# Optimization experiments

Hardware: AMD Instinct MI355X
Metric: run time of the kernel (lower is better)

The kernel has to match this reference:

```python
import jax, jax.numpy as jnp
import numpy as np

BLK = 64          # BLOCK_M == BLOCK_N == 64
TOPK_RATIO = 0.25


def _block_map(q, k, topk):
    # mean_pool of q blocks and mean-centered k blocks, then top-k key blocks per query block
    B, H, L, D = q.shape
    nb = L // BLK
    k_cent = k - jnp.mean(k, axis=-2, keepdims=True)
    pq = q.reshape(B, H, nb, BLK, D).mean(axis=3)          # [B,H,Mb,D]
    pk = k_cent.reshape(B, H, nb, BLK, D).mean(axis=3)     # [B,H,Nb,D]
    score = jnp.einsum('bhmd,bhnd->bhmn', pq, pk)
    _, lut = jax.lax.top_k(score, topk)                    # [B,H,Mb,topk] int32
    return lut


def reference(q, k, v):
    B, H, L, D = q.shape
    nb = L // BLK                       # M_BLOCKS == N_BLOCKS (L divisible by 64)
    topk = min(nb, int(TOPK_RATIO * nb))
    qk_scale = D ** (-0.5)

    lut = jax.lax.stop_gradient(_block_map(q, k, topk))    # routing is non-differentiable

    qb = q.reshape(B, H, nb, BLK, D)
    kb = k.reshape(B, H, nb, BLK, D)
    vb = v.reshape(B, H, nb, BLK, D)

    # gather selected key/value blocks per query block: [B,H,Mb,topk,BLK,D]
    idx = lut[:, :, :, :, None, None]
    k_sel = jnp.take_along_axis(kb[:, :, None], idx, axis=3)
    v_sel = jnp.take_along_axis(vb[:, :, None], idx, axis=3)

    # block-sparse attention restricted to the selected blocks
    s = jnp.einsum('bhmqd,bhmtkd->bhmqtk', qb, k_sel) * qk_scale
    s = s.reshape(B, H, nb, BLK, topk * BLK)
    p = jax.nn.softmax(s, axis=-1)                         # online-softmax equivalent
    v_flat = v_sel.reshape(B, H, nb, topk * BLK, D)
    o = jnp.einsum('bhmqn,bhmnd->bhmqd', p, v_flat)
    return o.reshape(B, H, L, D)


def setup_inputs() -> dict:
    key = jax.random.key(0)
    k1, k2, k3 = jax.random.split(key, 3)
    shape = (2, 8, 4096, 64)
    return {
        'q': jax.random.normal(k1, shape, dtype=jnp.float32),
        'k': jax.random.normal(k2, shape, dtype=jnp.float32),
        'v': jax.random.normal(k3, shape, dtype=jnp.float32),
    }
```

## Files before the change

kernel.cpp:

```cpp
#include <hip/hip_runtime.h>
#include <hip/hip_bf16.h>

#define B_ 2
#define H_ 8
#define L_ 4096
#define D_ 64
#define NB_ 64
#define TOPK_ 16
#define BH_ 16

typedef __bf16 bf16x8 __attribute__((ext_vector_type(8)));
typedef float f32x4 __attribute__((ext_vector_type(4)));

#if __has_builtin(__builtin_amdgcn_exp2f)
#define EXP2(x) __builtin_amdgcn_exp2f(x)
#else
#define EXP2(x) exp2f(x)
#endif

__global__ __launch_bounds__(256) void prep_all_kernel(
    const float* __restrict__ q, const float* __restrict__ k,
    const float* __restrict__ v,
    float* __restrict__ pq, float* __restrict__ pk,
    __bf16* __restrict__ kimg, __bf16* __restrict__ vimg) {
  const int tid = threadIdx.x;
  if (blockIdx.x < BH_ * NB_) {
    const int blk = blockIdx.x;
    const int bh = blk >> 6, m = blk & 63;
    const int d = tid & 63, g = tid >> 6;
    const float* qb = q + ((size_t)bh * L_ + m * 64 + g * 16) * D_ + d;
    float sq = 0.f;
#pragma unroll
    for (int i = 0; i < 16; i++) sq += qb[(size_t)i * D_];
    __shared__ float bufq[4][64];
    bufq[g][d] = sq;
    __syncthreads();
    if (g == 0) {
      float tq = bufq[0][d] + bufq[1][d] + bufq[2][d] + bufq[3][d];
      pq[(size_t)blk * 64 + d] = tq * (1.f / 64.f);
    }
  } else if (blockIdx.x < 2 * BH_ * NB_) {
    const int blk = blockIdx.x - BH_ * NB_;
    const int srow = tid >> 2;
    const int sc16 = (tid & 3) * 16;
    __shared__ __align__(16) float s_kf[64][64];
    __shared__ __align__(16) __bf16 s_kt[4096];

    const float* ks = k + (size_t)blk * 4096 + srow * 64 + sc16;
    float kf[16];
#pragma unroll
    for (int h = 0; h < 4; h++) {
      float4 t4 = *(const float4*)(ks + h * 4);
      kf[h * 4 + 0] = t4.x; kf[h * 4 + 1] = t4.y; kf[h * 4 + 2] = t4.z; kf[h * 4 + 3] = t4.w;
      *(float4*)&s_kf[srow][sc16 + h * 4] = t4;
    }

#pragma unroll
    for (int h = 0; h < 2; h++) {
      const int d0 = sc16 + h * 8;
      const int i = (d0 >> 5) * 4 + (srow >> 4);
      const int ln = ((d0 >> 3) & 3) * 16 + (srow & 15);
      bf16x8 kw;
#pragma unroll
      for (int j = 0; j < 8; j++) kw[j] = (__bf16)kf[h * 8 + j];
      *(bf16x8*)&s_kt[(i * 64 + ln) * 8] = kw;
    }
    __syncthreads();

    __bf16* gk = kimg + (size_t)blk * 4096;
    *(bf16x8*)(gk + tid * 8)        = *(const bf16x8*)(s_kt + tid * 8);
    *(bf16x8*)(gk + 2048 + tid * 8) = *(const bf16x8*)(s_kt + 2048 + tid * 8);

    const int d = tid & 63, g = tid >> 6;
    float sk = 0.f;
#pragma unroll
    for (int i = 0; i < 16; i++) sk += s_kf[g * 16 + i][d];
    __shared__ float bufk[4][64];
    bufk[g][d] = sk;
    __syncthreads();
    if (g == 0) {
      float tk = bufk[0][d] + bufk[1][d] + bufk[2][d] + bufk[3][d];
      pk[(size_t)blk * 64 + d] = tk * (1.f / 64.f);
    }
  } else {
    const int blk = blockIdx.x - 2 * BH_ * NB_;
    const int srow = tid >> 2;
    const int sc16 = (tid & 3) * 16;

    const float* vs = v + (size_t)blk * 4096 + srow * 64 + sc16;
    float vf[16];
#pragma unroll
    for (int h = 0; h < 4; h++) {
      float4 u4 = *(const float4*)(vs + h * 4);
      vf[h * 4 + 0] = u4.x; vf[h * 4 + 1] = u4.y; vf[h * 4 + 2] = u4.z; vf[h * 4 + 3] = u4.w;
    }

    const int kpos = (srow & 32) + ((srow >> 2) & 3) * 8 + ((srow >> 4) & 1) * 4 + (srow & 3);
    __shared__ __align__(16) __bf16 s_vt[4096];
#pragma unroll
    for (int i = 0; i < 16; i++) {
      int d = sc16 + i;
      s_vt[d * 64 + kpos] = (__bf16)vf[i];
    }
    __syncthreads();
    __bf16* gv = vimg + (size_t)blk * 4096;
#pragma unroll
    for (int h = 0; h < 2; h++) {
      int c = tid + h * 256;
      int i = c >> 6, ln = c & 63;
      int ct2 = i & 3, s2 = i >> 2;
      int d = ct2 * 16 + (ln & 15), c8 = s2 * 4 + (ln >> 4);
      *(bf16x8*)(gv + c * 8) = *(const bf16x8*)(s_vt + d * 64 + c8 * 8);
    }
  }
}

__global__ __launch_bounds__(256) void blockmap_kernel(
    const float* __restrict__ pq, const float* __restrict__ pk,
    int* __restrict__ lut) {
  const int g = blockIdx.x;
  const int bh = g >> 2, q4 = g & 3;
  const int t = threadIdx.x;
  const int lane = t & 63, w = t >> 6;

  __shared__ float s_pk[64][65];
  __shared__ float s_km[64];
  __shared__ float s_pq[16][64];
  __shared__ float s_sc[4][64];

#pragma unroll
  for (int i = 0; i < 16; i++) {
    int idx = i * 256 + t;
    s_pk[idx >> 6][idx & 63] = pk[(size_t)bh * 4096 + idx];
  }
#pragma unroll
  for (int i = 0; i < 4; i++) {
    int idx = i * 256 + t;
    s_pq[idx >> 6][idx & 63] = pq[(size_t)bh * 4096 + q4 * 1024 + idx];
  }
  __syncthreads();
  if (t < 64) {
    float s = 0.f;
#pragma unroll 8
    for (int r = 0; r < 64; r++) s += s_pk[r][t];
    s_km[t] = s * (1.f / 64.f);
  }
  __syncthreads();

#pragma unroll
  for (int rr = 0; rr < 4; rr++) {
    const int row = w * 4 + rr;
    float sc = 0.f;
#pragma unroll 8
    for (int d2 = 0; d2 < 64; ++d2)
      sc += s_pq[row][d2] * (s_pk[lane][d2] - s_km[d2]);
    s_sc[w][lane] = sc;
    __syncthreads();
    int rank = 0;
#pragma unroll 8
    for (int j = 0; j < 64; j++) {
      float o = s_sc[w][j];
      rank += (o > sc) || (o == sc && j < lane);
    }
    if (rank < TOPK_)
      lut[((size_t)bh * 64 + q4 * 16 + row) * TOPK_ + rank] = lane;
    __syncthreads();
  }
}

__global__ __launch_bounds__(256, 4) void sparse_attn_fast(
    const float* __restrict__ q, const __bf16* __restrict__ kimg,
    const __bf16* __restrict__ vimg, const float* __restrict__ pq,
    const float* __restrict__ pk, float* __restrict__ out) {
  const int bid = blockIdx.x;
  const int blk = (bid & 7) * 128 + (bid >> 3);
  const int bh = blk >> 6, m = blk & 63;
  const int tid = threadIdx.x;
  const int lane = tid & 63;
  const int w = tid >> 6;
  const int l16 = lane & 15, lhi = lane >> 4;

  __shared__ float s_pk[64][65];
  __shared__ float s_km[64];
  __shared__ float s_pqr[64];
  __shared__ float s_sc[64];
  __shared__ int s_lut[TOPK_];

  {
    const float* pkb = pk + (size_t)bh * 4096;
#pragma unroll
    for (int i = 0; i < 16; i++) {
      int idx = i * 256 + tid;
      s_pk[idx >> 6][idx & 63] = pkb[idx];
    }
    if (tid < 64) s_pqr[tid] = pq[((size_t)bh * 64 + m) * 64 + tid];
    __syncthreads();
    if (tid < 64) {
      float s = 0.f;
#pragma unroll 8
      for (int r = 0; r < 64; r++) s += s_pk[r][tid];
      s_km[tid] = s * (1.f / 64.f);
    }
    __syncthreads();
    float sc = 0.f;
#pragma unroll 8
    for (int d2 = 0; d2 < 64; ++d2)
      sc += s_pqr[d2] * (s_pk[lane][d2] - s_km[d2]);
    s_sc[lane] = sc;
    __syncthreads();
    int rank = 0;
#pragma unroll 8
    for (int j = 0; j < 64; j++) {
      float o = s_sc[j];
      rank += (o > sc) || (o == sc && j < lane);
    }
    if (rank < TOPK_) s_lut[rank] = lane;
    __syncthreads();
  }

  const size_t base = (size_t)bh * L_ * D_;
  const __bf16* kbase = kimg + (size_t)bh * 64 * 4096;
  const __bf16* vbase = vimg + (size_t)bh * 64 * 4096;

  const float QSC = 0.125f * 1.44269504088896340736f;
  bf16x8 qf[2];
  {
    const float* qrow = q + base + (size_t)(m * 64 + w * 16 + l16) * D_;
#pragma unroll
    for (int s = 0; s < 2; s++) {
      const float* p0 = qrow + s * 32 + lhi * 8;
      float4 a = *(const float4*)p0;
      float4 b = *(const float4*)(p0 + 4);
      bf16x8 f;
      f[0] = (__bf16)(a.x * QSC); f[1] = (__bf16)(a.y * QSC);
      f[2] = (__bf16)(a.z * QSC); f[3] = (__bf16)(a.w * QSC);
      f[4] = (__bf16)(b.x * QSC); f[5] = (__bf16)(b.y * QSC);
      f[6] = (__bf16)(b.z * QSC); f[7] = (__bf16)(b.w * QSC);
      qf[s] = f;
    }
  }

  f32x4 acc_o[4];
#pragma unroll
  for (int i = 0; i < 4; i++) acc_o[i] = (f32x4){0.f, 0.f, 0.f, 0.f};
  float l_run = 0.f;

  for (int it = 0; it < TOPK_; ++it) {
    const int kb = s_lut[it];

    const __bf16* gk = kbase + (size_t)kb * 4096 + lane * 8;
    const __bf16* gv = vbase + (size_t)kb * 4096 + lane * 8;
    bf16x8 kf[8], vf[8];
#pragma unroll
    for (int j = 0; j < 8; j++) kf[j] = *(const bf16x8*)(gk + j * 512);
#pragma unroll
    for (int j = 0; j < 8; j++) vf[j] = *(const bf16x8*)(gv + j * 512);

    f32x4 accs[4];
#pragma unroll
    for (int x = 0; x < 4; x++) accs[x] = (f32x4){0.f, 0.f, 0.f, 0.f};
    __builtin_amdgcn_s_setprio(1);
#pragma unroll
    for (int ct = 0; ct < 4; ct++) {
#pragma unroll
      for (int s = 0; s < 2; s++)
        accs[ct] = __builtin_amdgcn_mfma_f32_16x16x32_bf16(kf[s * 4 + ct], qf[s], accs[ct], 0, 0, 0);
    }
    __builtin_amdgcn_s_setprio(0);

    bf16x8 pa0, pa1;
    float ls0 = 0.f, ls1 = 0.f;
#pragma unroll
    for (int j = 0; j < 8; j++) {
      float e0 = EXP2(accs[(j >> 2)][j & 3]);
      float e1 = EXP2(accs[2 + (j >> 2)][j & 3]);
      pa0[j] = (__bf16)e0; pa1[j] = (__bf16)e1;
      ls0 += e0; ls1 += e1;
    }
    l_run += ls0 + ls1;

    __builtin_amdgcn_s_setprio(1);
#pragma unroll
    for (int ct2 = 0; ct2 < 4; ct2++) {
      acc_o[ct2] = __builtin_amdgcn_mfma_f32_16x16x32_bf16(pa0, vf[ct2], acc_o[ct2], 0, 0, 0);
      acc_o[ct2] = __builtin_amdgcn_mfma_f32_16x16x32_bf16(pa1, vf[4 + ct2], acc_o[ct2], 0, 0, 0);
    }
    __builtin_amdgcn_s_setprio(0);
  }

  l_run += __shfl_xor(l_run, 16, 64);
  l_run += __shfl_xor(l_run, 32, 64);
  float rq[4];
#pragma unroll
  for (int r = 0; r < 4; r++)
    rq[r] = 1.f / __shfl(l_run, (lane & 48) | (lhi * 4 + r), 64);

  float* ob = out + base + (size_t)(m * 64 + w * 16) * D_;
#pragma unroll
  for (int ct2 = 0; ct2 < 4; ct2++) {
#pragma unroll
    for (int r = 0; r < 4; r++) {
      const int row = lhi * 4 + r, col = ct2 * 16 + l16;
      ob[(size_t)row * D_ + col] = acc_o[ct2][r] * rq[r];
    }
  }
}

__global__ __launch_bounds__(256) void block_means_kernel(
    const float* __restrict__ q, const float* __restrict__ k,
    float* __restrict__ pq, float* __restrict__ pk) {
  const int blk = blockIdx.x;
  const int bh = blk >> 6, m = blk & 63;
  const int d = threadIdx.x & 63, g = threadIdx.x >> 6;
  const float* qb = q + ((size_t)bh * L_ + m * 64 + g * 16) * D_ + d;
  const float* kb = k + ((size_t)bh * L_ + m * 64 + g * 16) * D_ + d;
  float sq = 0.f, sk = 0.f;
#pragma unroll
  for (int i = 0; i < 16; i++) { sq += qb[(size_t)i * D_]; sk += kb[(size_t)i * D_]; }
  __shared__ float bufq[4][64];
  __shared__ float bufk[4][64];
  bufq[g][d] = sq; bufk[g][d] = sk;
  __syncthreads();
  if (g == 0) {
    float tq = bufq[0][d] + bufq[1][d] + bufq[2][d] + bufq[3][d];
    float tk = bufk[0][d] + bufk[1][d] + bufk[2][d] + bufk[3][d];
    pq[(size_t)blk * 64 + d] = tq * (1.f / 64.f);
    pk[(size_t)blk * 64 + d] = tk * (1.f / 64.f);
  }
}

__global__ __launch_bounds__(256) void sparse_attn_slow(
    const float* __restrict__ q, const float* __restrict__ k,
    const float* __restrict__ v, const int* __restrict__ lut,
    float* __restrict__ out) {
  const int blk = blockIdx.x;
  const int bh = blk >> 6, m = blk & 63;
  const int tid = threadIdx.x;
  const int lane = tid & 63;
  const int w = tid >> 6;
  const int l16 = lane & 15, lhi = lane >> 4;

  __shared__ __align__(16) __bf16 Kl[64 * 64];
  __shared__ __align__(16) __bf16 Vt[64 * 64];
  __shared__ __align__(16) __bf16 Pl[4][16 * 64];

  const size_t base = (size_t)bh * L_ * D_;

  bf16x8 qf[2];
  {
    const float* qrow = q + base + (size_t)(m * 64 + w * 16 + l16) * D_;
#pragma unroll
    for (int s = 0; s < 2; s++) {
      const float* p0 = qrow + s * 32 + lhi * 8;
      float4 a = *(const float4*)p0;
      float4 b = *(const float4*)(p0 + 4);
      bf16x8 f;
      f[0] = (__bf16)(a.x * 0.125f); f[1] = (__bf16)(a.y * 0.125f);
      f[2] = (__bf16)(a.z * 0.125f); f[3] = (__bf16)(a.w * 0.125f);
      f[4] = (__bf16)(b.x * 0.125f); f[5] = (__bf16)(b.y * 0.125f);
      f[6] = (__bf16)(b.z * 0.125f); f[7] = (__bf16)(b.w * 0.125f);
      qf[s] = f;
    }
  }

  f32x4 acc_o[4];
#pragma unroll
  for (int i = 0; i < 4; i++) acc_o[i] = (f32x4){0.f, 0.f, 0.f, 0.f};
  float m_run[4] = {-__builtin_inff(), -__builtin_inff(), -__builtin_inff(), -__builtin_inff()};
  float l_run[4] = {0.f, 0.f, 0.f, 0.f};

  const int srow = tid >> 2;
  const int sc16 = (tid & 3) * 16;

  for (int it = 0; it < TOPK_; ++it) {
    const int kb = lut[(size_t)blk * TOPK_ + it];
    __syncthreads();
    {
      const float* ks = k + base + (size_t)(kb * 64 + srow) * D_ + sc16;
      const float* vs = v + base + (size_t)(kb * 64 + srow) * D_ + sc16;
      float kf[16], vf[16];
#pragma unroll
      for (int h = 0; h < 4; h++) {
        float4 t4 = *(const float4*)(ks + h * 4);
        kf[h * 4 + 0] = t4.x; kf[h * 4 + 1] = t4.y; kf[h * 4 + 2] = t4.z; kf[h * 4 + 3] = t4.w;
        float4 u4 = *(const float4*)(vs + h * 4);
        vf[h * 4 + 0] = u4.x; vf[h * 4 + 1] = u4.y; vf[h * 4 + 2] = u4.z; vf[h * 4 + 3] = u4.w;
      }
#pragma unroll
      for (int h = 0; h < 2; h++) {
        int c8 = (sc16 >> 3) + h;
        bf16x8 kw;
#pragma unroll
        for (int j = 0; j < 8; j++) kw[j] = (__bf16)kf[h * 8 + j];
        *(bf16x8*)&Kl[srow * 64 + ((c8 ^ (srow & 7)) << 3)] = kw;
      }
#pragma unroll
      for (int i = 0; i < 16; i++) {
        int d = sc16 + i;
        Vt[d * 64 + (srow ^ ((d & 7) << 3))] = (__bf16)vf[i];
      }
    }
    __syncthreads();

    f32x4 accs[4];
#pragma unroll
    for (int i = 0; i < 4; i++) accs[i] = (f32x4){0.f, 0.f, 0.f, 0.f};
#pragma unroll
    for (int ct = 0; ct < 4; ct++) {
      const int key = ct * 16 + l16;
#pragma unroll
      for (int s = 0; s < 2; s++) {
        const int c8 = s * 4 + lhi;
        bf16x8 bk = *(const bf16x8*)&Kl[key * 64 + ((c8 ^ (key & 7)) << 3)];
        accs[ct] = __builtin_amdgcn_mfma_f32_16x16x32_bf16(qf[s], bk, accs[ct], 0, 0, 0);
      }
    }

    float pvals[4][4];
#pragma unroll
    for (int r = 0; r < 4; r++) {
      float mx = fmaxf(fmaxf(accs[0][r], accs[1][r]), fmaxf(accs[2][r], accs[3][r]));
#pragma unroll
      for (int off = 1; off < 16; off <<= 1) mx = fmaxf(mx, __shfl_xor(mx, off, 64));
      const float mnew = fmaxf(m_run[r], mx);
      const float scale = __expf(m_run[r] - mnew);
      float rs = 0.f;
#pragma unroll
      for (int ct = 0; ct < 4; ct++) {
        float e = __expf(accs[ct][r] - mnew);
        pvals[ct][r] = e; rs += e;
      }
#pragma unroll
      for (int off = 1; off < 16; off <<= 1) rs += __shfl_xor(rs, off, 64);
      l_run[r] = l_run[r] * scale + rs;
      m_run[r] = mnew;
#pragma unroll
      for (int ct = 0; ct < 4; ct++) acc_o[ct][r] *= scale;
    }

#pragma unroll
    for (int ct = 0; ct < 4; ct++) {
#pragma unroll
      for (int r = 0; r < 4; r++) {
        const int row = lhi * 4 + r, col = ct * 16 + l16;
        Pl[w][row * 64 + (col ^ ((row & 7) << 3))] = (__bf16)pvals[ct][r];
      }
    }
#pragma unroll
    for (int s = 0; s < 2; s++) {
      const int c8 = s * 4 + lhi;
      bf16x8 pa = *(const bf16x8*)&Pl[w][l16 * 64 + ((c8 ^ (l16 & 7)) << 3)];
#pragma unroll
      for (int ct2 = 0; ct2 < 4; ct2++) {
        const int d = ct2 * 16 + l16;
        bf16x8 bv = *(const bf16x8*)&Vt[d * 64 + ((c8 ^ (d & 7)) << 3)];
        acc_o[ct2] = __builtin_amdgcn_mfma_f32_16x16x32_bf16(pa, bv, acc_o[ct2], 0, 0, 0);
      }
    }
  }

  float* ob = out + base + (size_t)(m * 64 + w * 16) * D_;
#pragma unroll
  for (int ct2 = 0; ct2 < 4; ct2++) {
#pragma unroll
    for (int r = 0; r < 4; r++) {
      const int row = lhi * 4 + r, col = ct2 * 16 + l16;
      ob[(size_t)row * D_ + col] = acc_o[ct2][r] / l_run[r];
    }
  }
}

extern "C" void kernel_launch(void* const* d_in, const int* in_sizes, int n_in,
                              void* d_out, int out_size, void* d_ws, size_t ws_size,
                              hipStream_t stream) {
  const float* q = (const float*)d_in[0];
  const float* k = (const float*)d_in[1];
  const float* v = (const float*)d_in[2];
  float* out = (float*)d_out;

  float* pq = (float*)d_ws;
  float* pk = pq + (size_t)BH_ * NB_ * D_;
  int*   lut = (int*)(pk + (size_t)BH_ * NB_ * D_);
  char*  extra = (char*)(lut + (size_t)BH_ * NB_ * TOPK_);
  __bf16* kimg = (__bf16*)extra;
  __bf16* vimg = kimg + (size_t)BH_ * NB_ * 4096;

  const size_t needed = (size_t)((char*)(vimg + (size_t)BH_ * NB_ * 4096) - (char*)d_ws);
  const bool fast = ws_size >= needed;

  if (fast) {
    hipLaunchKernelGGL(prep_all_kernel, dim3(3 * BH_ * NB_), dim3(256), 0, stream,
                       q, k, v, pq, pk, kimg, vimg);
    hipLaunchKernelGGL(sparse_attn_fast, dim3(BH_ * NB_), dim3(256), 0, stream,
                       q, kimg, vimg, pq, pk, out);
  } else {
    hipLaunchKernelGGL(block_means_kernel, dim3(BH_ * NB_), dim3(256), 0, stream, q, k, pq, pk);
    hipLaunchKernelGGL(blockmap_kernel, dim3(BH_ * 4), dim3(256), 0, stream, pq, pk, lut);
    hipLaunchKernelGGL(sparse_attn_slow, dim3(BH_ * NB_), dim3(256), 0, stream, q, k, v, lut, out);
  }
}
```

Measured before the change: 54.45 us.

## Stage K/V blocks into LDS with async double-buffered copies and swizzled layout

Before, each wave loaded the selected K/V blocks straight from global memory into registers, so all four waves fetched the same data redundantly. Now the 256 threads share the work and copy each block once into a double-buffered LDS area with global_load_lds, prefetching the next block while the current one is computed. The prep kernel writes K and transposed V in an XOR-swizzled layout so MFMA operands can be read from LDS without bank conflicts. The cost is 32KB of LDS per block, two barriers per iteration, and the removal of the occupancy hint from launch bounds.

```diff
diff --git a/kernel.cpp b/kernel.cpp
--- a/kernel.cpp
+++ b/kernel.cpp
@@ -18,11 +18,17 @@
 #define EXP2(x) exp2f(x)
 #endif
 
+__device__ __forceinline__ void async_copy16(void* lds, const void* g) {
+  __builtin_amdgcn_global_load_lds(
+      (const __attribute__((address_space(1))) void*)g,
+      (__attribute__((address_space(3))) void*)lds, 16, 0, 0);
+}
+
 __global__ __launch_bounds__(256) void prep_all_kernel(
     const float* __restrict__ q, const float* __restrict__ k,
     const float* __restrict__ v,
     float* __restrict__ pq, float* __restrict__ pk,
-    __bf16* __restrict__ kimg, __bf16* __restrict__ vimg) {
+    __bf16* __restrict__ kswz, __bf16* __restrict__ vtswz) {
   const int tid = threadIdx.x;
   if (blockIdx.x < BH_ * NB_) {
     const int blk = blockIdx.x;
@@ -44,7 +50,6 @@
     const int srow = tid >> 2;
     const int sc16 = (tid & 3) * 16;
     __shared__ __align__(16) float s_kf[64][64];
-    __shared__ __align__(16) __bf16 s_kt[4096];
 
     const float* ks = k + (size_t)blk * 4096 + srow * 64 + sc16;
     float kf[16];
@@ -55,21 +60,16 @@
       *(float4*)&s_kf[srow][sc16 + h * 4] = t4;
     }
 
+    __bf16* gk = kswz + (size_t)blk * 4096;
 #pragma unroll
     for (int h = 0; h < 2; h++) {
-      const int d0 = sc16 + h * 8;
-      const int i = (d0 >> 5) * 4 + (srow >> 4);
-      const int ln = ((d0 >> 3) & 3) * 16 + (srow & 15);
+      int c8 = (sc16 >> 3) + h;
       bf16x8 kw;
 #pragma unroll
       for (int j = 0; j < 8; j++) kw[j] = (__bf16)kf[h * 8 + j];
-      *(bf16x8*)&s_kt[(i * 64 + ln) * 8] = kw;
-    }
-    __syncthreads();
-
-    __bf16* gk = kimg + (size_t)blk * 4096;
-    *(bf16x8*)(gk + tid * 8)        = *(const bf16x8*)(s_kt + tid * 8);
-    *(bf16x8*)(gk + 2048 + tid * 8) = *(const bf16x8*)(s_kt + 2048 + tid * 8);
+      *(bf16x8*)(gk + srow * 64 + ((c8 ^ (srow & 7)) << 3)) = kw;
+    }
+    __syncthreads();
 
     const int d = tid & 63, g = tid >> 6;
     float sk = 0.f;
@@ -100,18 +100,12 @@
 #pragma unroll
     for (int i = 0; i < 16; i++) {
       int d = sc16 + i;
-      s_vt[d * 64 + kpos] = (__bf16)vf[i];
-    }
-    __syncthreads();
-    __bf16* gv = vimg + (size_t)blk * 4096;
-#pragma unroll
-    for (int h = 0; h < 2; h++) {
-      int c = tid + h * 256;
-      int i = c >> 6, ln = c & 63;
-      int ct2 = i & 3, s2 = i >> 2;
-      int d = ct2 * 16 + (ln & 15), c8 = s2 * 4 + (ln >> 4);
-      *(bf16x8*)(gv + c * 8) = *(const bf16x8*)(s_vt + d * 64 + c8 * 8);
-    }
+      s_vt[d * 64 + (kpos ^ ((d & 7) << 3))] = (__bf16)vf[i];
+    }
+    __syncthreads();
+    __bf16* gv = vtswz + (size_t)blk * 4096;
+    *(bf16x8*)(gv + tid * 8)        = *(const bf16x8*)(s_vt + tid * 8);
+    *(bf16x8*)(gv + 2048 + tid * 8) = *(const bf16x8*)(s_vt + 2048 + tid * 8);
   }
 }
 
@@ -168,9 +162,9 @@
   }
 }
 
-__global__ __launch_bounds__(256, 4) void sparse_attn_fast(
-    const float* __restrict__ q, const __bf16* __restrict__ kimg,
-    const __bf16* __restrict__ vimg, const float* __restrict__ pq,
+__global__ __launch_bounds__(256) void sparse_attn_fast(
+    const float* __restrict__ q, const __bf16* __restrict__ kswz,
+    const __bf16* __restrict__ vtswz, const float* __restrict__ pq,
     const float* __restrict__ pk, float* __restrict__ out) {
   const int bid = blockIdx.x;
   const int blk = (bid & 7) * 128 + (bid >> 3);
@@ -180,13 +174,14 @@
   const int w = tid >> 6;
   const int l16 = lane & 15, lhi = lane >> 4;
 
-  __shared__ float s_pk[64][65];
+  __shared__ __align__(16) __bf16 KV[2][8192];
   __shared__ float s_km[64];
   __shared__ float s_pqr[64];
   __shared__ float s_sc[64];
   __shared__ int s_lut[TOPK_];
 
   {
+    float (*s_pk)[65] = (float(*)[65]) & KV[0][0];
     const float* pkb = pk + (size_t)bh * 4096;
 #pragma unroll
     for (int i = 0; i < 16; i++) {
@@ -219,8 +214,8 @@
   }
 
   const size_t base = (size_t)bh * L_ * D_;
-  const __bf16* kbase = kimg + (size_t)bh * 64 * 4096;
-  const __bf16* vbase = vimg + (size_t)bh * 64 * 4096;
+  const __bf16* kimg = kswz + (size_t)bh * 64 * 4096;
+  const __bf16* vbase = vtswz + (size_t)bh * 64 * 4096;
 
   const float QSC = 0.125f * 1.44269504088896340736f;
   bf16x8 qf[2];
@@ -245,16 +240,30 @@
   for (int i = 0; i < 4; i++) acc_o[i] = (f32x4){0.f, 0.f, 0.f, 0.f};
   float l_run = 0.f;
 
+  auto stage = [&](int b, int kb) {
+    const __bf16* gk = kimg + (size_t)kb * 4096;
+    const __bf16* gv = vbase + (size_t)kb * 4096;
+    async_copy16(&KV[b][0 * 2048 + w * 512], gk + 0 * 2048 + tid * 8);
+    async_copy16(&KV[b][1 * 2048 + w * 512], gk + 1 * 2048 + tid * 8);
+    async_copy16(&KV[b][4096 + 0 * 2048 + w * 512], gv + 0 * 2048 + tid * 8);
+    async_copy16(&KV[b][4096 + 1 * 2048 + w * 512], gv + 1 * 2048 + tid * 8);
+  };
+
+  stage(0, s_lut[0]);
+
   for (int it = 0; it < TOPK_; ++it) {
-    const int kb = s_lut[it];
-
-    const __bf16* gk = kbase + (size_t)kb * 4096 + lane * 8;
-    const __bf16* gv = vbase + (size_t)kb * 4096 + lane * 8;
-    bf16x8 kf[8], vf[8];
-#pragma unroll
-    for (int j = 0; j < 8; j++) kf[j] = *(const bf16x8*)(gk + j * 512);
-#pragma unroll
-    for (int j = 0; j < 8; j++) vf[j] = *(const bf16x8*)(gv + j * 512);
+    const int cur = it & 1;
+    if (it + 1 < TOPK_) {
+      stage(cur ^ 1, s_lut[it + 1]);
+      asm volatile("s_waitcnt vmcnt(4)" ::: "memory");
+    } else {
+      asm volatile("s_waitcnt vmcnt(0)" ::: "memory");
+    }
+    __builtin_amdgcn_s_barrier();
+    __builtin_amdgcn_sched_barrier(0);
+
+    const __bf16* Kl = &KV[cur][0];
+    const __bf16* Vt = &KV[cur][4096];
 
     f32x4 accs[4];
 #pragma unroll
@@ -262,9 +271,13 @@
     __builtin_amdgcn_s_setprio(1);
 #pragma unroll
     for (int ct = 0; ct < 4; ct++) {
-#pragma unroll
-      for (int s = 0; s < 2; s++)
-        accs[ct] = __builtin_amdgcn_mfma_f32_16x16x32_bf16(kf[s * 4 + ct], qf[s], accs[ct], 0, 0, 0);
+      const int key = ct * 16 + l16;
+#pragma unroll
+      for (int s = 0; s < 2; s++) {
+        const int c8 = s * 4 + lhi;
+        bf16x8 bk = *(const bf16x8*)&Kl[key * 64 + ((c8 ^ (key & 7)) << 3)];
+        accs[ct] = __builtin_amdgcn_mfma_f32_16x16x32_bf16(bk, qf[s], accs[ct], 0, 0, 0);
+      }
     }
     __builtin_amdgcn_s_setprio(0);
 
@@ -281,11 +294,19 @@
 
     __builtin_amdgcn_s_setprio(1);
 #pragma unroll
-    for (int ct2 = 0; ct2 < 4; ct2++) {
-      acc_o[ct2] = __builtin_amdgcn_mfma_f32_16x16x32_bf16(pa0, vf[ct2], acc_o[ct2], 0, 0, 0);
-      acc_o[ct2] = __builtin_amdgcn_mfma_f32_16x16x32_bf16(pa1, vf[4 + ct2], acc_o[ct2], 0, 0, 0);
+    for (int s2 = 0; s2 < 2; s2++) {
+      const int c8 = s2 * 4 + lhi;
+      const bf16x8 pa = s2 ? pa1 : pa0;
+#pragma unroll
+      for (int ct2 = 0; ct2 < 4; ct2++) {
+        const int d = ct2 * 16 + l16;
+        bf16x8 bv = *(const bf16x8*)&Vt[d * 64 + ((c8 ^ (d & 7)) << 3)];
+        acc_o[ct2] = __builtin_amdgcn_mfma_f32_16x16x32_bf16(pa, bv, acc_o[ct2], 0, 0, 0);
+      }
     }
     __builtin_amdgcn_s_setprio(0);
+
+    __builtin_amdgcn_s_barrier();
   }
 
   l_run += __shfl_xor(l_run, 16, 64);
@@ -482,17 +503,17 @@
   float* pk = pq + (size_t)BH_ * NB_ * D_;
   int*   lut = (int*)(pk + (size_t)BH_ * NB_ * D_);
   char*  extra = (char*)(lut + (size_t)BH_ * NB_ * TOPK_);
-  __bf16* kimg = (__bf16*)extra;
-  __bf16* vimg = kimg + (size_t)BH_ * NB_ * 4096;
-
-  const size_t needed = (size_t)((char*)(vimg + (size_t)BH_ * NB_ * 4096) - (char*)d_ws);
+  __bf16* kswz = (__bf16*)extra;
+  __bf16* vtswz = kswz + (size_t)BH_ * NB_ * 4096;
+
+  const size_t needed = (size_t)((char*)(vtswz + (size_t)BH_ * NB_ * 4096) - (char*)d_ws);
   const bool fast = ws_size >= needed;
 
   if (fast) {
     hipLaunchKernelGGL(prep_all_kernel, dim3(3 * BH_ * NB_), dim3(256), 0, stream,
-                       q, k, v, pq, pk, kimg, vimg);
+                       q, k, v, pq, pk, kswz, vtswz);
     hipLaunchKernelGGL(sparse_attn_fast, dim3(BH_ * NB_), dim3(256), 0, stream,
-                       q, kimg, vimg, pq, pk, out);
+                       q, kswz, vtswz, pq, pk, out);
   } else {
     hipLaunchKernelGGL(block_means_kernel, dim3(BH_ * NB_), dim3(256), 0, stream, q, k, pq, pk);
     hipLaunchKernelGGL(blockmap_kernel, dim3(BH_ * 4), dim3(256), 0, stream, pq, pk, lut);
```

Measured after the change: 48.21 us. 1.13x faster.
